# Kernel optimization log

Measured on AMD Instinct MI355X. Metric: run time of the kernel, lower is better.

The kernel has to match this reference:

```python
import jax, jax.numpy as jnp
import numpy as np

DIM = 2048
STATE = 2048
SEL_H = 1024
B = 16384


def setup_inputs() -> dict:
    key = jax.random.key(0)
    ks = jax.random.split(key, 7)
    def lin(k, out_f, in_f):
        return jax.random.normal(k, (out_f, in_f), dtype=jnp.float32) / np.sqrt(in_f)
    return {
        "x_t": jax.random.normal(ks[0], (B, DIM), dtype=jnp.float32),
        "h_prev": jax.random.normal(ks[1], (B, STATE), dtype=jnp.float32),
        "W_in": lin(ks[2], STATE, DIM),
        "W_sel_in": lin(ks[3], SEL_H, DIM),
        "W_sel_out": lin(ks[4], 4 * STATE, SEL_H),
        "W_out": lin(ks[5], DIM, STATE),
        "d": jnp.ones((STATE,), dtype=jnp.float32),
    }


def reference(x_t, h_prev, W_in, W_sel_in, W_sel_out, W_out, d):
    # u_t = in_proj(x_t): [B, state]
    u_t = x_t @ W_in.T
    # selector: silu(x @ W_sel_in.T) @ W_sel_out.T -> [B, 4*state]
    sel_h = jax.nn.silu(x_t @ W_sel_in.T)
    sel = sel_h @ W_sel_out.T
    a_raw, b_raw, c_raw, d_raw = jnp.split(sel, 4, axis=-1)
    a_t = jax.nn.sigmoid(a_raw)
    b_t = jnp.tanh(b_raw)
    c_t = jnp.tanh(c_raw)
    d_t = jax.nn.sigmoid(d_raw)
    h_t = a_t * h_prev + b_t * u_t
    y_t = c_t * h_t + d[None, :] * d_t * u_t
    out = y_t @ W_out.T  # [B, dim]
    return (out, h_t)
```

## Files before the change

kernel.cpp:

```cpp
#include <hip/hip_runtime.h>
#include <hip/hip_bf16.h>
#include <cstdint>

#define NB    16384
#define DIMX  2048
#define STATE 2048
#define SELH  1024

typedef unsigned short u16;
typedef short  short8_t __attribute__((ext_vector_type(8)));
typedef float  f32x4    __attribute__((ext_vector_type(4)));

__device__ __forceinline__ u16 f2bf(float f) {
  unsigned u = __builtin_bit_cast(unsigned, f);
  u += 0x7fffu + ((u >> 16) & 1u);
  return (u16)(u >> 16);
}
__device__ __forceinline__ float bf2f(u16 h) {
  unsigned u = ((unsigned)h) << 16;
  return __builtin_bit_cast(float, u);
}
__device__ __forceinline__ float sigmoidf_(float x) { return 1.f / (1.f + __expf(-x)); }
__device__ __forceinline__ float tanhf_(float x)    { return 2.f / (1.f + __expf(-2.f * x)) - 1.f; }

__device__ __forceinline__ f32x4 mfma_bf16(short8_t a, short8_t b, f32x4 c) {
  return __builtin_amdgcn_mfma_f32_16x16x32_bf16(a, b, c, 0, 0, 0);
}

__device__ __forceinline__ void gload16(const void* g, const void* l) {
  __builtin_amdgcn_global_load_lds(
      (const __attribute__((address_space(1))) unsigned int*)(uintptr_t)g,
      (__attribute__((address_space(3))) unsigned int*)(unsigned int)(uintptr_t)l,
      16, 0, 0);
}

#define LDS_V(p) (*(const short8_t*)__builtin_assume_aligned((const void*)(p), 16))

__global__ __launch_bounds__(256) void k_f32_to_bf16(const float* __restrict__ src,
                                                     u16* __restrict__ dst, int n4) {
  int i = blockIdx.x * blockDim.x + threadIdx.x;
  int stride = gridDim.x * blockDim.x;
  for (; i < n4; i += stride) {
    float4 v = ((const float4*)src)[i];
    ushort4 o;
    o.x = f2bf(v.x); o.y = f2bf(v.y); o.z = f2bf(v.z); o.w = f2bf(v.w);
    ((ushort4*)dst)[i] = o;
  }
}

template <int EPI, int KD, int NCOLS>
__global__ __launch_bounds__(512, 2) void k_gemm256(const u16* __restrict__ A,
                                                    const u16* __restrict__ Bsrc,
                                                    float* __restrict__ f32out,
                                                    u16* __restrict__ bfout,
                                                    const float* __restrict__ hprev,
                                                    const u16* __restrict__ ubf,
                                                    const float* __restrict__ dvec) {
  __shared__ __align__(16) char smem[131072];
  const int tid = threadIdx.x;
  const int w = tid >> 6, l = tid & 63;
  const int wr = w >> 2, wc = w & 3;
  const int bx = blockIdx.x, by = blockIdx.y;
  const int m0 = by * 256;

  const unsigned aAddr0 = (unsigned)(wr * 16384 + (l & 15) * 128 +
                                     (((l >> 4) * 16) ^ ((l & 7) << 4)));
  const unsigned aAddr1 = aAddr0 ^ 64u;
  const unsigned bAddr0 = (unsigned)(65536 + (wc * 64 + (l & 15)) * 64 +
                                     (((l >> 4) * 16) ^ ((l & 3) << 4)));
  const unsigned bAddr1 = bAddr0 + 16384u;

  const int rA = tid >> 3;
  const int kA = ((tid & 7) ^ ((tid >> 3) & 7)) * 8;
  const u16* aSrc = A + (size_t)(m0 + rA) * KD + kA;

  const int rB = tid >> 2;
  const int kB = ((tid & 3) ^ ((tid >> 2) & 3)) * 8;
  size_t bRow0, bRow1;
  if constexpr (EPI <= 2) {
    bRow0 = (size_t)bx * 256 + rB;
    bRow1 = bRow0 + 128;
  } else {
    const int s0 = bx * 64;
    const int r1 = rB + 128;
    bRow0 = (size_t)((rB >> 4) & 3) * STATE + s0 + (rB >> 6) * 16 + (rB & 15);
    bRow1 = (size_t)((r1 >> 4) & 3) * STATE + s0 + (r1 >> 6) * 16 + (r1 & 15);
  }
  const u16* bSrc0 = Bsrc + bRow0 * KD + kB;
  const u16* bSrc1 = Bsrc + bRow1 * KD + kB;

  auto stageA = [&](int k0n, int rh, unsigned dstD) {
    const u16* sp = aSrc + (size_t)rh * 128 * KD + k0n;
    gload16(sp,           smem + dstD + (unsigned)rh * 16384u + (unsigned)tid * 16u);
    gload16(sp + 64 * KD, smem + dstD + (unsigned)rh * 16384u + 8192u + (unsigned)tid * 16u);
  };
  auto stageB = [&](int k0n, int kh, unsigned dstD) {
    const int kk = k0n + kh * 32;
    gload16(bSrc0 + kk, smem + 65536u + dstD + (unsigned)kh * 16384u + (unsigned)tid * 16u);
    gload16(bSrc1 + kk, smem + 65536u + dstD + (unsigned)kh * 16384u + 8192u + (unsigned)tid * 16u);
  };

  f32x4 acc[8][4];
#pragma unroll
  for (int i = 0; i < 8; ++i)
#pragma unroll
    for (int j = 0; j < 4; ++j) acc[i][j] = f32x4{0.f, 0.f, 0.f, 0.f};

  short8_t ava[8], avb[8], bv01a[2], bv23a[2], bv23b[2], bv01b[2];

#define KTILE(D, DO_STAGE, K0N, LASTT)                                         \
  {                                                                            \
                                                        \
    if (LASTT) { asm volatile("s_waitcnt vmcnt(0)" ::: "memory"); }            \
    else       { asm volatile("s_waitcnt vmcnt(2)" ::: "memory"); }            \
    __builtin_amdgcn_s_barrier();                                              \
    __builtin_amdgcn_sched_barrier(0);                                         \
    bv01a[0] = LDS_V(smem + bAddr0 + (D) * 32768u);                            \
    bv01a[1] = LDS_V(smem + bAddr0 + (D) * 32768u + 1024u);                    \
    _Pragma("unroll") for (int mf = 0; mf < 8; ++mf)                           \
        ava[mf] = LDS_V(smem + aAddr0 + (D) * 32768u + mf * 2048u);            \
    if (DO_STAGE) { stageA(K0N, 0, (D ^ 1) * 32768u);                          \
                    stageA(K0N, 1, (D ^ 1) * 32768u); }                        \
    __builtin_amdgcn_s_setprio(1);                                             \
    _Pragma("unroll") for (int mf = 0; mf < 8; ++mf) {                         \
      acc[mf][0] = mfma_bf16(ava[mf], bv01a[0], acc[mf][0]);                   \
      acc[mf][1] = mfma_bf16(ava[mf], bv01a[1], acc[mf][1]);                   \
    }                                                                          \
    __builtin_amdgcn_s_setprio(0);                                             \
                                                                       \
    if (LASTT) { asm volatile("s_waitcnt vmcnt(0)" ::: "memory"); }            \
    else       { asm volatile("s_waitcnt vmcnt(4)" ::: "memory"); }            \
    __builtin_amdgcn_s_barrier();                                              \
    __builtin_amdgcn_sched_barrier(0);                                         \
    bv23a[0] = LDS_V(smem + bAddr0 + (D) * 32768u + 2048u);                    \
    bv23a[1] = LDS_V(smem + bAddr0 + (D) * 32768u + 3072u);                    \
    bv23b[0] = LDS_V(smem + bAddr1 + (D) * 32768u + 2048u);                    \
    bv23b[1] = LDS_V(smem + bAddr1 + (D) * 32768u + 3072u);                    \
    _Pragma("unroll") for (int mf = 0; mf < 8; ++mf)                           \
        avb[mf] = LDS_V(smem + aAddr1 + (D) * 32768u + mf * 2048u);            \
    if (DO_STAGE) { stageB(K0N, 0, (D ^ 1) * 32768u);                          \
                    stageB(K0N, 1, (D ^ 1) * 32768u); }                        \
    __builtin_amdgcn_s_setprio(1);                                             \
    _Pragma("unroll") for (int mf = 0; mf < 8; ++mf) {                         \
      acc[mf][2] = mfma_bf16(ava[mf], bv23a[0], acc[mf][2]);                   \
      acc[mf][3] = mfma_bf16(ava[mf], bv23a[1], acc[mf][3]);                   \
    }                                                                          \
    __builtin_amdgcn_s_setprio(0);                                             \
                                                          \
    bv01b[0] = LDS_V(smem + bAddr1 + (D) * 32768u);                            \
    bv01b[1] = LDS_V(smem + bAddr1 + (D) * 32768u + 1024u);                    \
    __builtin_amdgcn_s_setprio(1);                                             \
    _Pragma("unroll") for (int mf = 0; mf < 8; ++mf) {                         \
      acc[mf][2] = mfma_bf16(avb[mf], bv23b[0], acc[mf][2]);                   \
      acc[mf][3] = mfma_bf16(avb[mf], bv23b[1], acc[mf][3]);                   \
    }                                                                          \
    __builtin_amdgcn_s_setprio(0);                                             \
                                                          \
    __builtin_amdgcn_s_setprio(1);                                             \
    _Pragma("unroll") for (int mf = 0; mf < 8; ++mf) {                         \
      acc[mf][0] = mfma_bf16(avb[mf], bv01b[0], acc[mf][0]);                   \
      acc[mf][1] = mfma_bf16(avb[mf], bv01b[1], acc[mf][1]);                   \
    }                                                                          \
    __builtin_amdgcn_s_setprio(0);                                             \
  }

  stageA(0, 0, 0u); stageA(0, 1, 0u); stageB(0, 0, 0u); stageB(0, 1, 0u);

  constexpr int NT = KD / 64;
  int k0 = 0;
#pragma unroll 1
  for (int T = 0; T < NT - 2; T += 2) {
    KTILE(0, true, k0 + 64, false);
    KTILE(1, true, k0 + 128, false);
    k0 += 128;
  }
  KTILE(0, true, k0 + 64, false);
  KTILE(1, false, 0, true);

#undef KTILE

  const int rbase = m0 + wr * 128 + ((l >> 4) << 2);
  if constexpr (EPI <= 2) {
    const int cbase = bx * 256 + wc * 64 + (l & 15);
#pragma unroll
    for (int mf = 0; mf < 8; ++mf)
#pragma unroll
      for (int nf = 0; nf < 4; ++nf)
#pragma unroll
        for (int r = 0; r < 4; ++r) {
          const int row = rbase + mf * 16 + r;
          const int col = cbase + nf * 16;
          const size_t idx = (size_t)row * NCOLS + col;
          const float v = acc[mf][nf][r];
          if constexpr (EPI == 0) {
            bfout[idx] = f2bf(v);
          } else if constexpr (EPI == 1) {
            bfout[idx] = f2bf(v * sigmoidf_(v));
          } else {
            f32out[idx] = v;
          }
        }
  } else {
    const int s = bx * 64 + wc * 16 + (l & 15);
    const float dval = dvec[s];
#pragma unroll
    for (int mf = 0; mf < 8; ++mf)
#pragma unroll
      for (int r = 0; r < 4; ++r) {
        const int row = rbase + mf * 16 + r;
        const size_t idx = (size_t)row * STATE + s;
        const float a  = acc[mf][0][r];
        const float b  = acc[mf][1][r];
        const float c  = acc[mf][2][r];
        const float dd = acc[mf][3][r];
        const float uu = bf2f(ubf[idx]);
        const float hp = hprev[idx];
        const float h = sigmoidf_(a) * hp + tanhf_(b) * uu;
        f32out[idx] = h;
        bfout[idx] = f2bf(tanhf_(c) * h + dval * sigmoidf_(dd) * uu);
      }
  }
}

extern "C" void kernel_launch(void* const* d_in, const int* in_sizes, int n_in,
                              void* d_out, int out_size, void* d_ws, size_t ws_size,
                              hipStream_t stream) {
  const float* x   = (const float*)d_in[0];
  const float* h0  = (const float*)d_in[1];
  const float* Win = (const float*)d_in[2];
  const float* Wsi = (const float*)d_in[3];
  const float* Wso = (const float*)d_in[4];
  const float* Wou = (const float*)d_in[5];
  const float* dv  = (const float*)d_in[6];
  float* out  = (float*)d_out;
  float* hout = out + (size_t)NB * DIMX;

  u16* ws = (u16*)d_ws;
  size_t o = 0;
  u16* xb   = ws + o; o += (size_t)NB * DIMX;
  u16* ub   = ws + o; o += (size_t)NB * STATE;
  u16* yb   = ws + o; o += (size_t)NB * STATE;
  u16* sh   = ws + o; o += (size_t)NB * SELH;
  u16* wib  = ws + o; o += (size_t)STATE * DIMX;
  u16* wsib = ws + o; o += (size_t)SELH * DIMX;
  u16* wsob = ws + o; o += (size_t)4 * STATE * SELH;
  u16* wob  = ws + o; o += (size_t)DIMX * STATE;

  k_f32_to_bf16<<<1024, 256, 0, stream>>>(x,   xb,   NB * DIMX / 4);
  k_f32_to_bf16<<<256,  256, 0, stream>>>(Win, wib,  STATE * DIMX / 4);
  k_f32_to_bf16<<<128,  256, 0, stream>>>(Wsi, wsib, SELH * DIMX / 4);
  k_f32_to_bf16<<<512,  256, 0, stream>>>(Wso, wsob, 4 * STATE * SELH / 4);
  k_f32_to_bf16<<<256,  256, 0, stream>>>(Wou, wob,  DIMX * STATE / 4);

  const dim3 blk(512);
  k_gemm256<0, DIMX, STATE><<<dim3(STATE / 256, NB / 256), blk, 0, stream>>>(
      xb, wib, nullptr, ub, nullptr, nullptr, nullptr);
  k_gemm256<1, DIMX, SELH><<<dim3(SELH / 256, NB / 256), blk, 0, stream>>>(
      xb, wsib, nullptr, sh, nullptr, nullptr, nullptr);
  k_gemm256<3, SELH, 0><<<dim3(STATE / 64, NB / 256), blk, 0, stream>>>(
      sh, wsob, hout, yb, h0, ub, dv);
  k_gemm256<2, STATE, DIMX><<<dim3(DIMX / 256, NB / 256), blk, 0, stream>>>(
      yb, wob, out, nullptr, nullptr, nullptr, nullptr);
}
```

Before: 755.7 us.

## Fuse in-proj and selector-in GEMMs and merge weight conversions into one launch

```diff
diff --git a/kernel.cpp b/kernel.cpp
--- a/kernel.cpp
+++ b/kernel.cpp
@@ -36,16 +36,22 @@
 
 #define LDS_V(p) (*(const short8_t*)__builtin_assume_aligned((const void*)(p), 16))
 
-__global__ __launch_bounds__(256) void k_f32_to_bf16(const float* __restrict__ src,
-                                                     u16* __restrict__ dst, int n4) {
-  int i = blockIdx.x * blockDim.x + threadIdx.x;
-  int stride = gridDim.x * blockDim.x;
-  for (; i < n4; i += stride) {
-    float4 v = ((const float4*)src)[i];
-    ushort4 o;
-    o.x = f2bf(v.x); o.y = f2bf(v.y); o.z = f2bf(v.z); o.w = f2bf(v.w);
-    ((ushort4*)dst)[i] = o;
-  }
+__global__ __launch_bounds__(256) void k_convert5(const float* __restrict__ s0, u16* __restrict__ d0, int n0,
+                                                  const float* __restrict__ s1, u16* __restrict__ d1, int n1,
+                                                  const float* __restrict__ s2, u16* __restrict__ d2, int n2,
+                                                  const float* __restrict__ s3, u16* __restrict__ d3, int n3,
+                                                  const float* __restrict__ s4, u16* __restrict__ d4, int n4) {
+  const int base = blockIdx.x * blockDim.x + threadIdx.x;
+  const int stride = gridDim.x * blockDim.x;
+#define SEG(S, D, N)                                                     \
+  for (int i = base; i < (N); i += stride) {                             \
+    float4 v = ((const float4*)(S))[i];                                  \
+    ushort4 o;                                                           \
+    o.x = f2bf(v.x); o.y = f2bf(v.y); o.z = f2bf(v.z); o.w = f2bf(v.w);  \
+    ((ushort4*)(D))[i] = o;                                              \
+  }
+  SEG(s0, d0, n0) SEG(s1, d1, n1) SEG(s2, d2, n2) SEG(s3, d3, n3) SEG(s4, d4, n4)
+#undef SEG
 }
 
 template <int EPI, int KD, int NCOLS>
@@ -55,7 +61,8 @@
                                                     u16* __restrict__ bfout,
                                                     const float* __restrict__ hprev,
                                                     const u16* __restrict__ ubf,
-                                                    const float* __restrict__ dvec) {
+                                                    const float* __restrict__ dvec,
+                                                    u16* __restrict__ bfout2) {
   __shared__ __align__(16) char smem[131072];
   const int tid = threadIdx.x;
   const int w = tid >> 6, l = tid & 63;
@@ -77,7 +84,7 @@
   const int rB = tid >> 2;
   const int kB = ((tid & 3) ^ ((tid >> 2) & 3)) * 8;
   size_t bRow0, bRow1;
-  if constexpr (EPI <= 2) {
+  if constexpr (EPI != 3) {
     bRow0 = (size_t)bx * 256 + rB;
     bRow1 = bRow0 + 128;
   } else {
@@ -180,7 +187,7 @@
 #undef KTILE
 
   const int rbase = m0 + wr * 128 + ((l >> 4) << 2);
-  if constexpr (EPI <= 2) {
+  if constexpr (EPI == 2) {
     const int cbase = bx * 256 + wc * 64 + (l & 15);
 #pragma unroll
     for (int mf = 0; mf < 8; ++mf)
@@ -190,16 +197,34 @@
         for (int r = 0; r < 4; ++r) {
           const int row = rbase + mf * 16 + r;
           const int col = cbase + nf * 16;
-          const size_t idx = (size_t)row * NCOLS + col;
-          const float v = acc[mf][nf][r];
-          if constexpr (EPI == 0) {
-            bfout[idx] = f2bf(v);
-          } else if constexpr (EPI == 1) {
-            bfout[idx] = f2bf(v * sigmoidf_(v));
-          } else {
-            f32out[idx] = v;
+          f32out[(size_t)row * NCOLS + col] = acc[mf][nf][r];
+        }
+  } else if constexpr (EPI == 5) {
+    const int cbase = bx * 256 + wc * 64 + (l & 15);
+    if (bx < STATE / 256) {
+#pragma unroll
+      for (int mf = 0; mf < 8; ++mf)
+#pragma unroll
+        for (int nf = 0; nf < 4; ++nf)
+#pragma unroll
+          for (int r = 0; r < 4; ++r) {
+            const int row = rbase + mf * 16 + r;
+            const int col = cbase + nf * 16;
+            bfout[(size_t)row * STATE + col] = f2bf(acc[mf][nf][r]);
           }
-        }
+    } else {
+#pragma unroll
+      for (int mf = 0; mf < 8; ++mf)
+#pragma unroll
+        for (int nf = 0; nf < 4; ++nf)
+#pragma unroll
+          for (int r = 0; r < 4; ++r) {
+            const int row = rbase + mf * 16 + r;
+            const int col = cbase + nf * 16 - STATE;
+            const float v = acc[mf][nf][r];
+            bfout2[(size_t)row * SELH + col] = f2bf(v * sigmoidf_(v));
+          }
+    }
   } else {
     const int s = bx * 64 + wc * 16 + (l & 15);
     const float dval = dvec[s];
@@ -246,19 +271,17 @@
   u16* wsob = ws + o; o += (size_t)4 * STATE * SELH;
   u16* wob  = ws + o; o += (size_t)DIMX * STATE;
 
-  k_f32_to_bf16<<<1024, 256, 0, stream>>>(x,   xb,   NB * DIMX / 4);
-  k_f32_to_bf16<<<256,  256, 0, stream>>>(Win, wib,  STATE * DIMX / 4);
-  k_f32_to_bf16<<<128,  256, 0, stream>>>(Wsi, wsib, SELH * DIMX / 4);
-  k_f32_to_bf16<<<512,  256, 0, stream>>>(Wso, wsob, 4 * STATE * SELH / 4);
-  k_f32_to_bf16<<<256,  256, 0, stream>>>(Wou, wob,  DIMX * STATE / 4);
+  k_convert5<<<2048, 256, 0, stream>>>(x,   xb,   NB * DIMX / 4,
+                                       Win, wib,  STATE * DIMX / 4,
+                                       Wsi, wsib, SELH * DIMX / 4,
+                                       Wso, wsob, 4 * STATE * SELH / 4,
+                                       Wou, wob,  DIMX * STATE / 4);
 
   const dim3 blk(512);
-  k_gemm256<0, DIMX, STATE><<<dim3(STATE / 256, NB / 256), blk, 0, stream>>>(
-      xb, wib, nullptr, ub, nullptr, nullptr, nullptr);
-  k_gemm256<1, DIMX, SELH><<<dim3(SELH / 256, NB / 256), blk, 0, stream>>>(
-      xb, wsib, nullptr, sh, nullptr, nullptr, nullptr);
+  k_gemm256<5, DIMX, 0><<<dim3((STATE + SELH) / 256, NB / 256), blk, 0, stream>>>(
+      xb, wib, nullptr, ub, nullptr, nullptr, nullptr, sh);
   k_gemm256<3, SELH, 0><<<dim3(STATE / 64, NB / 256), blk, 0, stream>>>(
-      sh, wsob, hout, yb, h0, ub, dv);
+      sh, wsob, hout, yb, h0, ub, dv, nullptr);
   k_gemm256<2, STATE, DIMX><<<dim3(DIMX / 256, NB / 256), blk, 0, stream>>>(
-      yb, wob, out, nullptr, nullptr, nullptr, nullptr);
-}
+      yb, wob, out, nullptr, nullptr, nullptr, nullptr, nullptr);
+}
```

Measured after the change: 717.0 us. -5.1%, faster.
